# Kernel tuning notes

Hardware: AMD Instinct MI355X
Metric: run time of the kernel (lower is better)

The kernel has to match this reference:

```python
import jax, jax.numpy as jnp
import numpy as np


def setup_inputs() -> dict:
    key = jax.random.key(0)
    k1, k2, k3 = jax.random.split(key, 3)
    B, D, R, O = 8192, 2048, 16, 64
    # small init scale so the 2048-step matrix chain product stays numerically sane
    inputs = jax.random.normal(k1, (B, D), dtype=jnp.float32) * 0.05
    # cores near identity (glorot-scale perturbation) to avoid chain blow-up/collapse
    cores = jnp.eye(R, dtype=jnp.float32)[None] + jax.random.normal(k2, (D, R, R), dtype=jnp.float32) * (1.0 / R)
    projection = jax.random.normal(k3, (R, O), dtype=jnp.float32) * (1.0 / np.sqrt(R))
    bias = jnp.zeros((O,), dtype=jnp.float32)
    return {"inputs": inputs, "cores": cores, "projection": projection, "bias": bias}


def reference(inputs, cores, projection, bias):
    # inputs: (B, D); cores: (D, R, R); projection: (R, O); bias: (O,)
    B = inputs.shape[0]
    R = cores.shape[-1]
    boundary0 = jnp.ones((B, R), dtype=inputs.dtype)  # MPS boundary vector

    x_t = inputs.T  # (D, B) so scan iterates over features

    def step(boundary, xs):
        core, x = xs  # core: (R, R), x: (B,)
        # boundary <- (boundary @ core) scaled by the feature value (A^i[x_i])
        boundary = jnp.matmul(boundary, core) * x[:, None]
        return boundary, None

    boundary, _ = jax.lax.scan(step, boundary0, (cores, x_t))
    out = jnp.matmul(boundary, projection) + bias  # (B, O)
    return out
```

## Files before the change

kernel.cpp:

```cpp
#include <hip/hip_runtime.h>
#include <math.h>


#define DFEAT 2048
#define R 16
#define NR2 256
#define OUTD 64
#define CHUNK 64
#define NCHUNK (DFEAT / CHUNK)
#define MAGIC 0x7E57C0DE

__device__ __forceinline__ float4 rowmul(const float* Arow, const float* B,
                                         int c0) {
    float4 acc = {0.f, 0.f, 0.f, 0.f};
    const float4* a4 = (const float4*)Arow;
#pragma unroll
    for (int kk = 0; kk < 4; ++kk) {
        const float4 av = a4[kk];
        const float4 b0 = *(const float4*)&B[(4 * kk + 0) * 16 + c0];
        const float4 b1 = *(const float4*)&B[(4 * kk + 1) * 16 + c0];
        const float4 b2 = *(const float4*)&B[(4 * kk + 2) * 16 + c0];
        const float4 b3 = *(const float4*)&B[(4 * kk + 3) * 16 + c0];
        acc.x = fmaf(av.x, b0.x, fmaf(av.y, b1.x, fmaf(av.z, b2.x, fmaf(av.w, b3.x, acc.x))));
        acc.y = fmaf(av.x, b0.y, fmaf(av.y, b1.y, fmaf(av.z, b2.y, fmaf(av.w, b3.y, acc.y))));
        acc.z = fmaf(av.x, b0.z, fmaf(av.y, b1.z, fmaf(av.z, b2.z, fmaf(av.w, b3.z, acc.z))));
        acc.w = fmaf(av.x, b0.w, fmaf(av.y, b1.w, fmaf(av.z, b2.w, fmaf(av.w, b3.w, acc.w))));
    }
    return acc;
}

__global__ __launch_bounds__(256) void mps_fused(const float* __restrict__ cores,
                                                 const float* __restrict__ proj,
                                                 const float* __restrict__ x,
                                                 float* __restrict__ prodbuf,
                                                 float* __restrict__ partials,
                                                 int* __restrict__ flags,
                                                 float* __restrict__ pE,
                                                 int B) {
    __shared__ __align__(16) float Bb[4][2][NR2];
    __shared__ __align__(16) float Aw[4][2][NR2];
    __shared__ __align__(16) float F[2][NR2];
    __shared__ __align__(16) float Pt[8 * NR2];

    const int tid  = threadIdx.x;
    const int wave = tid >> 6, lane = tid & 63;

    if (blockIdx.x >= NCHUNK) {
        const int row = (blockIdx.x - NCHUNK) * 4 + wave;
        if (row >= B) return;
        const float4* xr = (const float4*)(x + (size_t)row * DFEAT);
        float prod = 1.f;
#pragma unroll
        for (int it = 0; it < DFEAT / (64 * 4); ++it) {
            float4 v = xr[it * 64 + lane];
            prod *= (v.x * v.y) * (v.z * v.w);
        }
#pragma unroll
        for (int off = 32; off > 0; off >>= 1)
            prod *= __shfl_xor(prod, off);
        if (lane == 0) prodbuf[row] = prod;
        return;
    }

    const int ri = lane >> 2;
    const int c0 = (lane & 3) << 2;
    const size_t d0 = (size_t)blockIdx.x * CHUNK;

    const float* gw = cores + (d0 + 16 * wave) * NR2;
    float4 pre[16];
#pragma unroll
    for (int t = 0; t < 16; ++t)
        pre[t] = *(const float4*)&gw[(size_t)t * NR2 + lane * 4];

    *(float4*)&Aw[wave][0][lane * 4] = pre[0];
    int cur = 0;
#pragma unroll
    for (int t = 1; t < 16; ++t) {
        *(float4*)&Bb[wave][t & 1][lane * 4] = pre[t];
        float4 r = rowmul(&Aw[wave][cur][ri * 16], &Bb[wave][t & 1][0], c0);
        *(float4*)&Aw[wave][cur ^ 1][ri * 16 + c0] = r;
        cur ^= 1;
    }
    __syncthreads();

    if (wave == 0) {
        *(float4*)&F[0][ri * 16 + c0] =
            *(const float4*)&Aw[0][1][ri * 16 + c0];
        int cc = 0;
        for (int w = 1; w < 4; ++w) {
            float4 r = rowmul(&F[cc][ri * 16], &Aw[w][1][0], c0);
            *(float4*)&F[cc ^ 1][ri * 16 + c0] = r;
            cc ^= 1;
        }
    }
    __syncthreads();
    const int i = tid >> 4, j = tid & 15;
    const float v = F[1][tid];

    if (blockIdx.x != 0) {
        partials[blockIdx.x * NR2 + tid] = v;
        __syncthreads();
        if (tid == 0)
            __hip_atomic_store(&flags[blockIdx.x], MAGIC,
                               __ATOMIC_RELEASE, __HIP_MEMORY_SCOPE_AGENT);
        return;
    }

    Pt[0 * 256 + j * 16 + i] = v;

    {
        const int f = 1 + (tid % (NCHUNK - 1));
        while (__hip_atomic_load(&flags[f], __ATOMIC_ACQUIRE,
                                 __HIP_MEMORY_SCOPE_AGENT) != MAGIC) { }
    }
    __syncthreads();

    float w = 1.f;
    int E = 0;
    for (int rr = 0; rr < 4; ++rr) {
#pragma unroll
        for (int q = 0; q < 2; ++q) {
            const int idx = q * 256 + tid;
            const int flat = idx * 4;
            const int s = flat >> 8;
            if (rr > 0 || s > 0) {
                float4 p4 =
                    ((const float4*)(partials + (size_t)(8 * rr) * NR2))[idx];
                const int e = flat & 255;
                const int k = e >> 4, j0 = e & 15;
                Pt[s * 256 + (j0 + 0) * 16 + k] = p4.x;
                Pt[s * 256 + (j0 + 1) * 16 + k] = p4.y;
                Pt[s * 256 + (j0 + 2) * 16 + k] = p4.z;
                Pt[s * 256 + (j0 + 3) * 16 + k] = p4.w;
            }
        }
        __syncthreads();
        if (tid < 64) {
            const int jj = tid & 15, q = tid >> 4;
            for (int s = 0; s < 8; ++s) {
                const float4 pr = *(const float4*)&Pt[s * 256 + jj * 16 + 4 * q];
                float sum;
                sum = __shfl(w, 4 * q + 0) * pr.x;
                sum = fmaf(__shfl(w, 4 * q + 1), pr.y, sum);
                sum = fmaf(__shfl(w, 4 * q + 2), pr.z, sum);
                sum = fmaf(__shfl(w, 4 * q + 3), pr.w, sum);
                sum += __shfl_xor(sum, 16);
                sum += __shfl_xor(sum, 32);
                w = sum;
            }
            float m = fabsf(w);
#pragma unroll
            for (int off = 1; off <= 8; off <<= 1)
                m = fmaxf(m, __shfl_xor(m, off));
            if (m > 0.f) {
                int e2 = 0;
                (void)frexpf(m, &e2);
                w = ldexpf(w, -e2);
                E += e2;
            }
        }
        __syncthreads();
    }

    if (tid < 64) {
        float p = 0.f;
#pragma unroll
        for (int k = 0; k < R; ++k)
            p = fmaf(__shfl(w, k), proj[k * OUTD + tid], p);
        pE[tid] = p;
        if (tid == 0) ((int*)pE)[OUTD] = E;
    }
}

__global__ __launch_bounds__(256) void mps_scale(const float* __restrict__ prodbuf,
                                                 const float* __restrict__ pE,
                                                 const float* __restrict__ bias,
                                                 float* __restrict__ out,
                                                 int B) {
    const int gtid = blockIdx.x * 256 + threadIdx.x;
    const int row  = gtid >> 6;
    const int lane = threadIdx.x & 63;
    if (row >= B) return;
    const float pv = pE[lane];
    const int   E  = ((const int*)pE)[OUTD];
    out[(size_t)row * OUTD + lane] = ldexpf(pv * prodbuf[row], E) + bias[lane];
}

extern "C" void kernel_launch(void* const* d_in, const int* in_sizes, int n_in,
                              void* d_out, int out_size, void* d_ws, size_t ws_size,
                              hipStream_t stream) {
    const float* inputs = (const float*)d_in[0];
    const float* cores  = (const float*)d_in[1];
    const float* proj   = (const float*)d_in[2];
    const float* bias   = (const float*)d_in[3];
    float* out = (float*)d_out;

    const int B = in_sizes[0] / DFEAT;

    float* prodbuf  = (float*)d_ws;
    float* partials = prodbuf + B;
    float* pE    = partials + NCHUNK * NR2;
    int*   flags = (int*)(pE + 68);

    const int rowBlocks = (B + 3) / 4;
    mps_fused<<<NCHUNK + rowBlocks, 256, 0, stream>>>(cores, proj, inputs,
                                                      prodbuf, partials, flags,
                                                      pE, B);
    mps_scale<<<(B * 64 + 255) / 256, 256, 0, stream>>>(prodbuf, pE, bias,
                                                        out, B);
}
```

Baseline: 104.8 us.

## Merge scale kernel into a persistent cooperative kernel with grid sync

Replaces the two-kernel scheme with one cooperative launch of 512 persistent blocks. Chain blocks compute their partial products, streaming blocks loop over the row-product work, and after a grid-wide sync all blocks write the scaled output with float4 stores. This removes the second kernel launch and the per-row block oversubscription. In exchange it pays the cost of a grid barrier, cooperative-launch overhead, and less parallelism in the streaming phase.

Result: slower. 185.2 us (+76.7%).

```diff
diff --git a/kernel.cpp b/kernel.cpp
--- a/kernel.cpp
+++ b/kernel.cpp
@@ -1,6 +1,9 @@
 #include <hip/hip_runtime.h>
+#include <hip/hip_cooperative_groups.h>
 #include <math.h>
 
+
+namespace cg = cooperative_groups;
 
 #define DFEAT 2048
 #define R 16
@@ -9,6 +12,8 @@
 #define CHUNK 64
 #define NCHUNK (DFEAT / CHUNK)
 #define MAGIC 0x7E57C0DE
+#define NBLK 512
+#define NSTREAM (NBLK - NCHUNK)
 
 __device__ __forceinline__ float4 rowmul(const float* Arow, const float* B,
                                          int c0) {
@@ -29,14 +34,16 @@
     return acc;
 }
 
-__global__ __launch_bounds__(256) void mps_fused(const float* __restrict__ cores,
-                                                 const float* __restrict__ proj,
-                                                 const float* __restrict__ x,
-                                                 float* __restrict__ prodbuf,
-                                                 float* __restrict__ partials,
-                                                 int* __restrict__ flags,
-                                                 float* __restrict__ pE,
-                                                 int B) {
+__global__ __launch_bounds__(256) void mps_coop(const float* __restrict__ cores,
+                                                const float* __restrict__ proj,
+                                                const float* __restrict__ x,
+                                                const float* __restrict__ bias,
+                                                float* __restrict__ out,
+                                                float* __restrict__ prodbuf,
+                                                float* __restrict__ partials,
+                                                int* __restrict__ flags,
+                                                float* __restrict__ pE,
+                                                int B) {
     __shared__ __align__(16) float Bb[4][2][NR2];
     __shared__ __align__(16) float Aw[4][2][NR2];
     __shared__ __align__(16) float F[2][NR2];
@@ -44,146 +51,155 @@
 
     const int tid  = threadIdx.x;
     const int wave = tid >> 6, lane = tid & 63;
-
-    if (blockIdx.x >= NCHUNK) {
-        const int row = (blockIdx.x - NCHUNK) * 4 + wave;
-        if (row >= B) return;
-        const float4* xr = (const float4*)(x + (size_t)row * DFEAT);
-        float prod = 1.f;
-#pragma unroll
-        for (int it = 0; it < DFEAT / (64 * 4); ++it) {
-            float4 v = xr[it * 64 + lane];
-            prod *= (v.x * v.y) * (v.z * v.w);
-        }
-#pragma unroll
-        for (int off = 32; off > 0; off >>= 1)
-            prod *= __shfl_xor(prod, off);
-        if (lane == 0) prodbuf[row] = prod;
-        return;
+    const int bid  = blockIdx.x;
+
+    if (bid >= NCHUNK) {
+        const int nunits = B >> 2;
+        for (int u = bid - NCHUNK; u < nunits; u += NSTREAM) {
+            const int row = u * 4 + wave;
+            const float4* xr = (const float4*)(x + (size_t)row * DFEAT);
+            float prod = 1.f;
+#pragma unroll
+            for (int it = 0; it < DFEAT / (64 * 4); ++it) {
+                float4 v = xr[it * 64 + lane];
+                prod *= (v.x * v.y) * (v.z * v.w);
+            }
+#pragma unroll
+            for (int off = 32; off > 0; off >>= 1)
+                prod *= __shfl_xor(prod, off);
+            if (lane == 0) prodbuf[row] = prod;
+        }
+    } else {
+        const int ri = lane >> 2;
+        const int c0 = (lane & 3) << 2;
+        const size_t d0 = (size_t)bid * CHUNK;
+
+        const float* gw = cores + (d0 + 16 * wave) * NR2;
+        float4 pre[16];
+#pragma unroll
+        for (int t = 0; t < 16; ++t)
+            pre[t] = *(const float4*)&gw[(size_t)t * NR2 + lane * 4];
+
+        *(float4*)&Aw[wave][0][lane * 4] = pre[0];
+        int cur = 0;
+#pragma unroll
+        for (int t = 1; t < 16; ++t) {
+            *(float4*)&Bb[wave][t & 1][lane * 4] = pre[t];
+            float4 r = rowmul(&Aw[wave][cur][ri * 16], &Bb[wave][t & 1][0], c0);
+            *(float4*)&Aw[wave][cur ^ 1][ri * 16 + c0] = r;
+            cur ^= 1;
+        }
+        __syncthreads();
+
+        if (wave == 0) {
+            *(float4*)&F[0][ri * 16 + c0] =
+                *(const float4*)&Aw[0][1][ri * 16 + c0];
+            int cc = 0;
+            for (int w = 1; w < 4; ++w) {
+                float4 r = rowmul(&F[cc][ri * 16], &Aw[w][1][0], c0);
+                *(float4*)&F[cc ^ 1][ri * 16 + c0] = r;
+                cc ^= 1;
+            }
+        }
+        __syncthreads();
+        const int i = tid >> 4, j = tid & 15;
+        const float v = F[1][tid];
+
+        if (bid != 0) {
+            partials[bid * NR2 + tid] = v;
+            __syncthreads();
+            if (tid == 0)
+                __hip_atomic_store(&flags[bid], MAGIC,
+                                   __ATOMIC_RELEASE, __HIP_MEMORY_SCOPE_AGENT);
+        } else {
+            Pt[0 * 256 + j * 16 + i] = v;
+
+            {
+                const int f = 1 + (tid % (NCHUNK - 1));
+                while (__hip_atomic_load(&flags[f], __ATOMIC_ACQUIRE,
+                                         __HIP_MEMORY_SCOPE_AGENT) != MAGIC) { }
+            }
+            __syncthreads();
+
+            float w = 1.f;
+            int E = 0;
+            for (int rr = 0; rr < 4; ++rr) {
+#pragma unroll
+                for (int q = 0; q < 2; ++q) {
+                    const int idx = q * 256 + tid;
+                    const int flat = idx * 4;
+                    const int s = flat >> 8;
+                    if (rr > 0 || s > 0) {
+                        float4 p4 = ((const float4*)(partials +
+                                       (size_t)(8 * rr) * NR2))[idx];
+                        const int e = flat & 255;
+                        const int k = e >> 4, j0 = e & 15;
+                        Pt[s * 256 + (j0 + 0) * 16 + k] = p4.x;
+                        Pt[s * 256 + (j0 + 1) * 16 + k] = p4.y;
+                        Pt[s * 256 + (j0 + 2) * 16 + k] = p4.z;
+                        Pt[s * 256 + (j0 + 3) * 16 + k] = p4.w;
+                    }
+                }
+                __syncthreads();
+                if (tid < 64) {
+                    const int jj = tid & 15, q = tid >> 4;
+                    for (int s = 0; s < 8; ++s) {
+                        const float4 pr =
+                            *(const float4*)&Pt[s * 256 + jj * 16 + 4 * q];
+                        float sum;
+                        sum = __shfl(w, 4 * q + 0) * pr.x;
+                        sum = fmaf(__shfl(w, 4 * q + 1), pr.y, sum);
+                        sum = fmaf(__shfl(w, 4 * q + 2), pr.z, sum);
+                        sum = fmaf(__shfl(w, 4 * q + 3), pr.w, sum);
+                        sum += __shfl_xor(sum, 16);
+                        sum += __shfl_xor(sum, 32);
+                        w = sum;
+                    }
+                    float m = fabsf(w);
+#pragma unroll
+                    for (int off = 1; off <= 8; off <<= 1)
+                        m = fmaxf(m, __shfl_xor(m, off));
+                    if (m > 0.f) {
+                        int e2 = 0;
+                        (void)frexpf(m, &e2);
+                        w = ldexpf(w, -e2);
+                        E += e2;
+                    }
+                }
+                __syncthreads();
+            }
+
+            if (tid < 64) {
+                float p = 0.f;
+#pragma unroll
+                for (int k = 0; k < R; ++k)
+                    p = fmaf(__shfl(w, k), proj[k * OUTD + tid], p);
+                pE[tid] = p;
+                if (tid == 0) ((int*)pE)[OUTD] = E;
+            }
+        }
     }
 
-    const int ri = lane >> 2;
-    const int c0 = (lane & 3) << 2;
-    const size_t d0 = (size_t)blockIdx.x * CHUNK;
-
-    const float* gw = cores + (d0 + 16 * wave) * NR2;
-    float4 pre[16];
-#pragma unroll
-    for (int t = 0; t < 16; ++t)
-        pre[t] = *(const float4*)&gw[(size_t)t * NR2 + lane * 4];
-
-    *(float4*)&Aw[wave][0][lane * 4] = pre[0];
-    int cur = 0;
-#pragma unroll
-    for (int t = 1; t < 16; ++t) {
-        *(float4*)&Bb[wave][t & 1][lane * 4] = pre[t];
-        float4 r = rowmul(&Aw[wave][cur][ri * 16], &Bb[wave][t & 1][0], c0);
-        *(float4*)&Aw[wave][cur ^ 1][ri * 16 + c0] = r;
-        cur ^= 1;
+    cg::this_grid().sync();
+
+    const int E = ((const int*)pE)[OUTD];
+    const float4* pE4 = (const float4*)pE;
+    const float4* b4  = (const float4*)bias;
+    float4* o4 = (float4*)out;
+    const int total4 = B * (OUTD / 4);
+    for (int idx = bid * 256 + tid; idx < total4; idx += NBLK * 256) {
+        const int row = idx >> 4;
+        const int c4  = idx & 15;
+        const float pr = prodbuf[row];
+        const float4 pe = pE4[c4];
+        const float4 bb = b4[c4];
+        float4 r;
+        r.x = ldexpf(pe.x * pr, E) + bb.x;
+        r.y = ldexpf(pe.y * pr, E) + bb.y;
+        r.z = ldexpf(pe.z * pr, E) + bb.z;
+        r.w = ldexpf(pe.w * pr, E) + bb.w;
+        o4[idx] = r;
     }
-    __syncthreads();
-
-    if (wave == 0) {
-        *(float4*)&F[0][ri * 16 + c0] =
-            *(const float4*)&Aw[0][1][ri * 16 + c0];
-        int cc = 0;
-        for (int w = 1; w < 4; ++w) {
-            float4 r = rowmul(&F[cc][ri * 16], &Aw[w][1][0], c0);
-            *(float4*)&F[cc ^ 1][ri * 16 + c0] = r;
-            cc ^= 1;
-        }
-    }
-    __syncthreads();
-    const int i = tid >> 4, j = tid & 15;
-    const float v = F[1][tid];
-
-    if (blockIdx.x != 0) {
-        partials[blockIdx.x * NR2 + tid] = v;
-        __syncthreads();
-        if (tid == 0)
-            __hip_atomic_store(&flags[blockIdx.x], MAGIC,
-                               __ATOMIC_RELEASE, __HIP_MEMORY_SCOPE_AGENT);
-        return;
-    }
-
-    Pt[0 * 256 + j * 16 + i] = v;
-
-    {
-        const int f = 1 + (tid % (NCHUNK - 1));
-        while (__hip_atomic_load(&flags[f], __ATOMIC_ACQUIRE,
-                                 __HIP_MEMORY_SCOPE_AGENT) != MAGIC) { }
-    }
-    __syncthreads();
-
-    float w = 1.f;
-    int E = 0;
-    for (int rr = 0; rr < 4; ++rr) {
-#pragma unroll
-        for (int q = 0; q < 2; ++q) {
-            const int idx = q * 256 + tid;
-            const int flat = idx * 4;
-            const int s = flat >> 8;
-            if (rr > 0 || s > 0) {
-                float4 p4 =
-                    ((const float4*)(partials + (size_t)(8 * rr) * NR2))[idx];
-                const int e = flat & 255;
-                const int k = e >> 4, j0 = e & 15;
-                Pt[s * 256 + (j0 + 0) * 16 + k] = p4.x;
-                Pt[s * 256 + (j0 + 1) * 16 + k] = p4.y;
-                Pt[s * 256 + (j0 + 2) * 16 + k] = p4.z;
-                Pt[s * 256 + (j0 + 3) * 16 + k] = p4.w;
-            }
-        }
-        __syncthreads();
-        if (tid < 64) {
-            const int jj = tid & 15, q = tid >> 4;
-            for (int s = 0; s < 8; ++s) {
-                const float4 pr = *(const float4*)&Pt[s * 256 + jj * 16 + 4 * q];
-                float sum;
-                sum = __shfl(w, 4 * q + 0) * pr.x;
-                sum = fmaf(__shfl(w, 4 * q + 1), pr.y, sum);
-                sum = fmaf(__shfl(w, 4 * q + 2), pr.z, sum);
-                sum = fmaf(__shfl(w, 4 * q + 3), pr.w, sum);
-                sum += __shfl_xor(sum, 16);
-                sum += __shfl_xor(sum, 32);
-                w = sum;
-            }
-            float m = fabsf(w);
-#pragma unroll
-            for (int off = 1; off <= 8; off <<= 1)
-                m = fmaxf(m, __shfl_xor(m, off));
-            if (m > 0.f) {
-                int e2 = 0;
-                (void)frexpf(m, &e2);
-                w = ldexpf(w, -e2);
-                E += e2;
-            }
-        }
-        __syncthreads();
-    }
-
-    if (tid < 64) {
-        float p = 0.f;
-#pragma unroll
-        for (int k = 0; k < R; ++k)
-            p = fmaf(__shfl(w, k), proj[k * OUTD + tid], p);
-        pE[tid] = p;
-        if (tid == 0) ((int*)pE)[OUTD] = E;
-    }
-}
-
-__global__ __launch_bounds__(256) void mps_scale(const float* __restrict__ prodbuf,
-                                                 const float* __restrict__ pE,
-                                                 const float* __restrict__ bias,
-                                                 float* __restrict__ out,
-                                                 int B) {
-    const int gtid = blockIdx.x * 256 + threadIdx.x;
-    const int row  = gtid >> 6;
-    const int lane = threadIdx.x & 63;
-    if (row >= B) return;
-    const float pv = pE[lane];
-    const int   E  = ((const int*)pE)[OUTD];
-    out[(size_t)row * OUTD + lane] = ldexpf(pv * prodbuf[row], E) + bias[lane];
 }
 
 extern "C" void kernel_launch(void* const* d_in, const int* in_sizes, int n_in,
@@ -202,10 +218,9 @@
     float* pE    = partials + NCHUNK * NR2;
     int*   flags = (int*)(pE + 68);
 
-    const int rowBlocks = (B + 3) / 4;
-    mps_fused<<<NCHUNK + rowBlocks, 256, 0, stream>>>(cores, proj, inputs,
-                                                      prodbuf, partials, flags,
-                                                      pE, B);
-    mps_scale<<<(B * 64 + 255) / 256, 256, 0, stream>>>(prodbuf, pE, bias,
-                                                        out, B);
+    void* args[] = {(void*)&cores, (void*)&proj, (void*)&inputs, (void*)&bias,
+                    (void*)&out, (void*)&prodbuf, (void*)&partials,
+                    (void*)&flags, (void*)&pE, (void*)&B};
+    hipLaunchCooperativeKernel((const void*)mps_coop, dim3(NBLK), dim3(256),
+                               args, 0, stream);
 }
```
